# Optimization experiments

Measured on AMD Instinct MI355X. Metric: run time of the kernel, lower is better.

## Reference

```python
import jax, jax.numpy as jnp
import numpy as np
from jax import lax

NC1, NC2, NC3 = 64, 64, 512
TEMP = 1.0
EPS = 1e-5
B = 256


def setup_inputs() -> dict:
    key = jax.random.key(0)
    ks = jax.random.split(key, 16)
    d = {}
    d["inp"] = jax.random.normal(ks[0], (B, 3, 32, 32), jnp.float32)
    d["conv1_w"] = jax.random.normal(ks[1], (6, 3, 5, 5), jnp.float32) * 0.1
    d["conv1_b"] = jax.random.normal(ks[2], (6,), jnp.float32) * 0.1
    d["bn1_g"] = jnp.ones((6,), jnp.float32)
    d["bn1_b"] = jnp.zeros((6,), jnp.float32)
    d["conv2_w"] = jax.random.normal(ks[3], (16, 6, 5, 5), jnp.float32) * 0.1
    d["conv2_b"] = jax.random.normal(ks[4], (16,), jnp.float32) * 0.1
    d["bn2_g"] = jnp.ones((16,), jnp.float32)
    d["bn2_b"] = jnp.zeros((16,), jnp.float32)
    d["fc1_w"] = jax.random.normal(ks[5], (120, 400), jnp.float32) * 0.05
    d["fc1_b"] = jax.random.normal(ks[6], (120,), jnp.float32) * 0.05
    d["fc2_w"] = jax.random.normal(ks[7], (10, 120), jnp.float32) * 0.05
    d["fc2_b"] = jax.random.normal(ks[8], (10,), jnp.float32) * 0.05
    d["k1s"] = jax.random.normal(ks[9], (NC1, 6), jnp.float32)
    d["k2s"] = jax.random.normal(ks[10], (NC2, 16), jnp.float32)
    d["k3s"] = jax.random.normal(ks[11], (NC3, 120), jnp.float32)
    return d


def _conv(x, w, b):
    y = lax.conv_general_dilated(x, w, (1, 1), 'VALID',
                                 dimension_numbers=('NCHW', 'OIHW', 'NCHW'))
    return y + b[None, :, None, None]


def _bn_train(x, g, b):
    # BatchNorm2d in training mode: biased batch stats over (N,H,W)
    mean = x.mean(axis=(0, 2, 3), keepdims=True)
    var = ((x - mean) ** 2).mean(axis=(0, 2, 3), keepdims=True)
    return (x - mean) / jnp.sqrt(var + EPS) * g[None, :, None, None] + b[None, :, None, None]


def _maxpool2(x):
    return lax.reduce_window(x, -jnp.inf, lax.max, (1, 1, 2, 2), (1, 1, 2, 2), 'VALID')


def _codebook_logits_spatial(act, keys):
    # act: [B,C,H,W], keys: [K,C] -> -||act - k||_2 over C -> [B,K,H,W]
    diff = act[:, None] - keys[None, :, :, None, None]
    return -jnp.sqrt((diff ** 2).sum(axis=2))


def _neural_gas_loss(v, temp):
    n_clusters = v.shape[1]
    weightings = jnp.exp(-jnp.arange(n_clusters, dtype=v.dtype) / temp)
    sorted_v = jnp.sort(v, axis=1)
    return (sorted_v ** 2 * weightings).sum(axis=1)


def reference(inp, conv1_w, conv1_b, bn1_g, bn1_b, conv2_w, conv2_b, bn2_g, bn2_b,
              fc1_w, fc1_b, fc2_w, fc2_b, k1s, k2s, k3s):
    act1 = _bn_train(_conv(inp, conv1_w, conv1_b), bn1_g, bn1_b)          # [B,6,28,28]
    act_logits1 = _codebook_logits_spatial(act1, k1s)                     # [B,NC1,28,28]
    x = _maxpool2(jax.nn.relu(act1))                                      # [B,6,14,14]
    act2 = _bn_train(_conv(x, conv2_w, conv2_b), bn2_g, bn2_b)            # [B,16,10,10]
    act_logits2 = _codebook_logits_spatial(act2, k2s)                     # [B,NC2,10,10]
    x = _maxpool2(jax.nn.relu(act2))                                      # [B,16,5,5]
    x = x.reshape(x.shape[0], -1)                                         # [B,400]
    act3 = x @ fc1_w.T + fc1_b                                            # [B,120]
    diff3 = act3[:, None, :] - k3s[None, :, :]
    act_logits3 = -jnp.sqrt((diff3 ** 2).sum(axis=2))                     # [B,NC3]
    x = jax.nn.relu(act3)
    act4 = x @ fc2_w.T + fc2_b                                            # [B,10]
    # ARGS.ng branch: neural-gas cluster loss + argmax assignments
    cluster_loss = _neural_gas_loss(act_logits3, TEMP)                    # [B]
    assignments = jnp.argmax(act_logits3, axis=1)                         # [B] int
    return (assignments, cluster_loss.mean(), act4, act_logits1, act_logits2, act_logits3)
```

## Files before the change

kernel.cpp:

```cpp
#include <hip/hip_runtime.h>

#define B 256
#define EPSV 1e-5f

#define OFF_ASSIGN 0
#define OFF_LOSS   256
#define OFF_ACT4   257
#define OFF_L1     2817
#define OFF_L2     12847873
#define OFF_L3     14486273

__device__ inline void wave_reduce2(float& s, float& q) {
#pragma unroll
    for (int o = 32; o > 0; o >>= 1) {
        s += __shfl_down(s, o, 64);
        q += __shfl_down(q, o, 64);
    }
}

__global__ __launch_bounds__(256) void conv1_kernel(
        const float* __restrict__ inp, const float* __restrict__ w,
        const float* __restrict__ bias, float* __restrict__ c1,
        float* __restrict__ part,
        const float* __restrict__ w1, const float* __restrict__ k3,
        float* __restrict__ w1t, float* __restrict__ k3st) {
    int bc = blockIdx.x;
    int tid = threadIdx.x;
    if (bc >= 1536) {
        int idx = (bc - 1536) * 256 + tid;
        if (idx < 48000) {
            int c = idx / 120, o = idx % 120;
            w1t[idx] = w1[o * 400 + c];
        } else if (idx < 48000 + 61440) {
            int j = idx - 48000;
            int c = j >> 9, k = j & 511;
            k3st[j] = k3[k * 120 + c];
        }
        return;
    }
    int b = bc / 6, c = bc % 6;
    __shared__ float ws[75];
    __shared__ float rs[4], rq[4];
    if (tid < 75) ws[tid] = w[c * 75 + tid];
    __syncthreads();
    const float* ip = inp + b * 3072;
    float bs = bias[c];
    float s = 0.f, sq = 0.f;
    for (int hw = tid; hw < 784; hw += 256) {
        int oh = hw / 28, ow = hw % 28;
        float acc = bs;
#pragma unroll
        for (int ic = 0; ic < 3; ++ic) {
            const float* ipc = ip + ic * 1024 + oh * 32 + ow;
            const float* wc = ws + ic * 25;
#pragma unroll
            for (int kh = 0; kh < 5; ++kh)
#pragma unroll
                for (int kw = 0; kw < 5; ++kw)
                    acc += ipc[kh * 32 + kw] * wc[kh * 5 + kw];
        }
        c1[bc * 784 + hw] = acc;
        s += acc; sq += acc * acc;
    }
    wave_reduce2(s, sq);
    if ((tid & 63) == 0) { rs[tid >> 6] = s; rq[tid >> 6] = sq; }
    __syncthreads();
    if (tid == 0) {
        part[bc * 2]     = rs[0] + rs[1] + rs[2] + rs[3];
        part[bc * 2 + 1] = rq[0] + rq[1] + rq[2] + rq[3];
    }
}

__global__ __launch_bounds__(1024) void stage1_kernel(
        const float* __restrict__ c1raw, const float* __restrict__ part1,
        const float* __restrict__ g1, const float* __restrict__ bb1,
        const float* __restrict__ k1s,
        const float* __restrict__ c2w, const float* __restrict__ c2b,
        float* __restrict__ outL1, float* __restrict__ c2,
        float* __restrict__ part2) {
    int b = blockIdx.x, tid = threadIdx.x;
    int lane = tid & 63, wid = tid >> 6;
    __shared__ float act[4704];
    __shared__ float sk[384];
    __shared__ float w2s[2400];
    __shared__ float xp[1176];
    __shared__ float sa[1600];
    __shared__ float chs[6], chq[6], ssc[6], ssh[6];
    if (wid < 6) {
        float s = 0.f, q = 0.f;
#pragma unroll
        for (int j = 0; j < 4; ++j) {
            int bi = lane + 64 * j;
            s += part1[(bi * 6 + wid) * 2];
            q += part1[(bi * 6 + wid) * 2 + 1];
        }
        wave_reduce2(s, q);
        if (lane == 0) { chs[wid] = s; chq[wid] = q; }
    }
    for (int i = tid; i < 384; i += 1024) sk[i] = k1s[i];
    for (int i = tid; i < 2400; i += 1024) w2s[i] = c2w[i];
    __syncthreads();
    if (tid < 6) {
        float m = chs[tid] * (1.f / 200704.f);
        float v = chq[tid] * (1.f / 200704.f) - m * m;
        float sc = g1[tid] * rsqrtf(v + EPSV);
        ssc[tid] = sc; ssh[tid] = bb1[tid] - m * sc;
    }
    __syncthreads();
    const float* cp = c1raw + b * 4704;
    for (int i = tid; i < 4704; i += 1024) {
        int c = i / 784;
        act[i] = cp[i] * ssc[c] + ssh[c];
    }
    __syncthreads();
    float* op = outL1 + (long)b * 50176;
    for (int i = tid; i < 50176; i += 1024) {
        int k = i / 784, hw = i - k * 784;
        const float* kp = sk + k * 6;
        float d0 = act[hw] - kp[0];
        float d1 = act[784 + hw] - kp[1];
        float d2 = act[1568 + hw] - kp[2];
        float d3 = act[2352 + hw] - kp[3];
        float d4 = act[3136 + hw] - kp[4];
        float d5 = act[3920 + hw] - kp[5];
        float s = d0 * d0 + d1 * d1 + d2 * d2 + d3 * d3 + d4 * d4 + d5 * d5;
        op[i] = -sqrtf(s);
    }
    for (int i = tid; i < 1176; i += 1024) {
        int c = i / 196, p = i % 196, ph = p / 14, pw = p % 14;
        const float* ap = act + c * 784 + ph * 56 + pw * 2;
        float m = fmaxf(fmaxf(ap[0], ap[1]), fmaxf(ap[28], ap[29]));
        xp[i] = fmaxf(m, 0.f);
    }
    __syncthreads();
    for (int i = tid; i < 1600; i += 1024) {
        int c = i / 100, hw = i - c * 100;
        int oh = hw / 10, ow = hw - oh * 10;
        float acc = c2b[c];
#pragma unroll
        for (int ic = 0; ic < 6; ++ic) {
            const float* xsrc = xp + ic * 196 + oh * 14 + ow;
            const float* wp = w2s + c * 150 + ic * 25;
#pragma unroll
            for (int kh = 0; kh < 5; ++kh)
#pragma unroll
                for (int kw = 0; kw < 5; ++kw)
                    acc += xsrc[kh * 14 + kw] * wp[kh * 5 + kw];
        }
        sa[i] = acc;
    }
    __syncthreads();
    for (int i = tid; i < 1600; i += 1024) c2[b * 1600 + i] = sa[i];
    {
        float s = 0.f, q = 0.f;
        if (lane < 100) { float x = sa[wid * 100 + lane]; s = x; q = x * x; }
        if (lane < 36)  { float x = sa[wid * 100 + 64 + lane]; s += x; q += x * x; }
        wave_reduce2(s, q);
        if (lane == 0) {
            part2[(b * 16 + wid) * 2]     = s;
            part2[(b * 16 + wid) * 2 + 1] = q;
        }
    }
}

__global__ __launch_bounds__(1024) void stage2_kernel(
        const float* __restrict__ c2, const float* __restrict__ part2,
        const float* __restrict__ g2, const float* __restrict__ bb2,
        const float* __restrict__ k2s,
        const float* __restrict__ w1t, const float* __restrict__ f1b,
        const float* __restrict__ f2w, const float* __restrict__ f2b,
        const float* __restrict__ k3st,
        float* __restrict__ outL2, float* __restrict__ outAct4,
        float* __restrict__ outL3, float* __restrict__ outAssign,
        float* __restrict__ lossb) {
    int b = blockIdx.x, tid = threadIdx.x;
    int lane = tid & 63, wid = tid >> 6;
    __shared__ float sa[1600];
    __shared__ float sk[1024];
    __shared__ float xs[400];
    __shared__ float chs[16], chq[16], ssc[16], ssh[16];
    __shared__ float partq[8][128];
    __shared__ float a3r[120], a3p[120];
    __shared__ float pv[2][512];
    __shared__ float sv[512];
    __shared__ int   cntp[2][512];
    __shared__ float wsum[8], wmv[8];
    __shared__ int wmi[8];
    {
        float s = 0.f, q = 0.f;
#pragma unroll
        for (int j = 0; j < 4; ++j) {
            int bi = lane + 64 * j;
            s += part2[(bi * 16 + wid) * 2];
            q += part2[(bi * 16 + wid) * 2 + 1];
        }
        wave_reduce2(s, q);
        if (lane == 0) { chs[wid] = s; chq[wid] = q; }
    }
    for (int i = tid; i < 1024; i += 1024) sk[i] = k2s[i];
    __syncthreads();
    if (tid < 16) {
        float m = chs[tid] * (1.f / 25600.f);
        float v = chq[tid] * (1.f / 25600.f) - m * m;
        float sc = g2[tid] * rsqrtf(v + EPSV);
        ssc[tid] = sc; ssh[tid] = bb2[tid] - m * sc;
    }
    __syncthreads();
    for (int i = tid; i < 1600; i += 1024) {
        int c = i / 100;
        sa[i] = c2[b * 1600 + i] * ssc[c] + ssh[c];
    }
    __syncthreads();
    float* op2 = outL2 + (long)b * 6400;
    for (int i = tid; i < 6400; i += 1024) {
        int k = i / 100, hw = i - k * 100;
        float s = 0.f;
#pragma unroll
        for (int c = 0; c < 16; ++c) {
            float d = sa[c * 100 + hw] - sk[k * 16 + c];
            s += d * d;
        }
        op2[i] = -sqrtf(s);
    }
    for (int i = tid; i < 400; i += 1024) {
        int c = i / 25, p = i % 25, ph = p / 5, pw = p % 5;
        const float* ap = sa + c * 100 + ph * 20 + pw * 2;
        float m = fmaxf(fmaxf(ap[0], ap[1]), fmaxf(ap[10], ap[11]));
        xs[i] = fmaxf(m, 0.f);
    }
    __syncthreads();
    {
        int o = tid & 127, q8 = tid >> 7;
        float s = 0.f;
        if (o < 120) {
            const float* wp = w1t + (q8 * 50) * 120 + o;
            const float* xp2 = xs + q8 * 50;
#pragma unroll 10
            for (int c = 0; c < 50; ++c) s += xp2[c] * wp[c * 120];
        }
        partq[q8][o] = s;
    }
    __syncthreads();
    if (tid < 120) {
        float acc = f1b[tid];
#pragma unroll
        for (int q8 = 0; q8 < 8; ++q8) acc += partq[q8][tid];
        a3r[tid] = acc;
        a3p[tid] = fmaxf(acc, 0.f);
    }
    __syncthreads();
    {
        int k = tid & 511, h = tid >> 9;
        const float* kp = k3st + k;
        float s = 0.f;
#pragma unroll 10
        for (int c = 0; c < 60; ++c) {
            int cc = h * 60 + c;
            float d = a3r[cc] - kp[cc * 512];
            s += d * d;
        }
        pv[h][k] = s;
    }
    if (tid < 10) {
        float acc = f2b[tid];
        const float* wp = f2w + tid * 120;
#pragma unroll 8
        for (int c = 0; c < 120; ++c) acc += a3p[c] * wp[c];
        outAct4[b * 10 + tid] = acc;
    }
    __syncthreads();
    if (tid < 512) {
        float v = -sqrtf(pv[0][tid] + pv[1][tid]);
        sv[tid] = v;
        outL3[(long)b * 512 + tid] = v;
    }
    __syncthreads();
    {
        int i = tid & 511, h = tid >> 9;
        float v = sv[i];
        const float4* sv4 = reinterpret_cast<const float4*>(sv);
        int cnt = 0;
#pragma unroll 8
        for (int j4 = h * 64; j4 < h * 64 + 64; ++j4) {
            float4 o4 = sv4[j4];
            int jb = j4 * 4;
            cnt += (o4.x < v || (o4.x == v && jb < i)) ? 1 : 0;
            cnt += (o4.y < v || (o4.y == v && jb + 1 < i)) ? 1 : 0;
            cnt += (o4.z < v || (o4.z == v && jb + 2 < i)) ? 1 : 0;
            cnt += (o4.w < v || (o4.w == v && jb + 3 < i)) ? 1 : 0;
        }
        cntp[h][i] = cnt;
    }
    __syncthreads();
    if (tid < 512) {
        float v = sv[tid];
        int cnt = cntp[0][tid] + cntp[1][tid];
        float contrib = v * v * expf(-(float)cnt);
        float ssum = contrib;
#pragma unroll
        for (int o = 32; o > 0; o >>= 1) ssum += __shfl_down(ssum, o, 64);
        float mv = v; int mi = tid;
#pragma unroll
        for (int o = 32; o > 0; o >>= 1) {
            float ov = __shfl_down(mv, o, 64);
            int oi = __shfl_down(mi, o, 64);
            if (ov > mv || (ov == mv && oi < mi)) { mv = ov; mi = oi; }
        }
        if (lane == 0) { wsum[wid] = ssum; wmv[wid] = mv; wmi[wid] = mi; }
    }
    __syncthreads();
    if (tid == 0) {
        float tot = 0.f;
        float bmv = wmv[0]; int bmi = wmi[0];
#pragma unroll
        for (int w = 0; w < 8; ++w) {
            tot += wsum[w];
            if (wmv[w] > bmv || (wmv[w] == bmv && wmi[w] < bmi)) { bmv = wmv[w]; bmi = wmi[w]; }
        }
        lossb[b] = tot;
        outAssign[b] = (float)bmi;
    }
}

__global__ void final_kernel(const float* __restrict__ loss_b, float* __restrict__ out_loss) {
    __shared__ float r[256];
    int tid = threadIdx.x;
    r[tid] = loss_b[tid];
    __syncthreads();
    for (int s = 128; s > 0; s >>= 1) {
        if (tid < s) r[tid] += r[tid + s];
        __syncthreads();
    }
    if (tid == 0) out_loss[0] = r[0] / 256.f;
}

extern "C" void kernel_launch(void* const* d_in, const int* in_sizes, int n_in,
                              void* d_out, int out_size, void* d_ws, size_t ws_size,
                              hipStream_t stream) {
    const float* inp = (const float*)d_in[0];
    const float* c1w = (const float*)d_in[1];
    const float* c1b = (const float*)d_in[2];
    const float* g1  = (const float*)d_in[3];
    const float* bb1 = (const float*)d_in[4];
    const float* c2w = (const float*)d_in[5];
    const float* c2b = (const float*)d_in[6];
    const float* g2  = (const float*)d_in[7];
    const float* bb2 = (const float*)d_in[8];
    const float* f1w = (const float*)d_in[9];
    const float* f1b = (const float*)d_in[10];
    const float* f2w = (const float*)d_in[11];
    const float* f2b = (const float*)d_in[12];
    const float* k1  = (const float*)d_in[13];
    const float* k2  = (const float*)d_in[14];
    const float* k3  = (const float*)d_in[15];
    float* out = (float*)d_out;

    float* W = (float*)d_ws;
    float* c1raw = W;
    float* part1 = c1raw + 1204224;
    float* c2raw = part1 + 3072;
    float* part2 = c2raw + 409600;
    float* lossb = part2 + 8192;
    float* w1t   = lossb + 256;
    float* k3st  = w1t + 48000;

    conv1_kernel<<<1964, 256, 0, stream>>>(inp, c1w, c1b, c1raw, part1,
                                           f1w, k3, w1t, k3st);
    stage1_kernel<<<B, 1024, 0, stream>>>(c1raw, part1, g1, bb1, k1, c2w, c2b,
                                          out + OFF_L1, c2raw, part2);
    stage2_kernel<<<B, 1024, 0, stream>>>(c2raw, part2, g2, bb2, k2,
                                          w1t, f1b, f2w, f2b, k3st,
                                          out + OFF_L2, out + OFF_ACT4,
                                          out + OFF_L3, out + OFF_ASSIGN, lossb);
    final_kernel<<<1, 256, 0, stream>>>(lossb, out + OFF_LOSS);
}
```

Measured before the change: 94.49 us.

## Use norm expansion for codebook distances and overlap pooling with logit computation

Codebook distances are now computed as ||a||^2 + ||k||^2 - 2 a·k, clamped at zero. Each thread keeps one pixel's activations in registers and loops over the codebook entries, while a separate set of threads does the max-pooling at the same time. The conv2 output is written to global memory directly instead of in a second pass. This cuts per-element subtraction work and index division, and lets the pooling threads run alongside the logit threads. In exchange it may lose floating-point accuracy when distances are small, through cancellation, and each thread's stores now stride by plane instead of being fully contiguous across iterations.

Result: faster. 91.79 us (-2.9%).

```diff
diff --git a/kernel.cpp b/kernel.cpp
--- a/kernel.cpp
+++ b/kernel.cpp
@@ -10,7 +10,7 @@
 #define OFF_L2     12847873
 #define OFF_L3     14486273
 
-__device__ inline void wave_reduce2(float& s, float& q) {
+__device__ __forceinline__ void wave_reduce2(float& s, float& q) {
 #pragma unroll
     for (int o = 32; o > 0; o >>= 1) {
         s += __shfl_down(s, o, 64);
@@ -76,15 +76,15 @@
         const float* __restrict__ g1, const float* __restrict__ bb1,
         const float* __restrict__ k1s,
         const float* __restrict__ c2w, const float* __restrict__ c2b,
-        float* __restrict__ outL1, float* __restrict__ c2,
+        float* __restrict__ out, float* __restrict__ c2raw,
         float* __restrict__ part2) {
     int b = blockIdx.x, tid = threadIdx.x;
     int lane = tid & 63, wid = tid >> 6;
-    __shared__ float act[4704];
-    __shared__ float sk[384];
+    __shared__ __align__(16) float act[4704];
+    __shared__ float sk1[384], k2sq1[64];
     __shared__ float w2s[2400];
     __shared__ float xp[1176];
-    __shared__ float sa[1600];
+    __shared__ __align__(16) float sa[1600];
     __shared__ float chs[6], chq[6], ssc[6], ssh[6];
     if (wid < 6) {
         float s = 0.f, q = 0.f;
@@ -97,7 +97,7 @@
         wave_reduce2(s, q);
         if (lane == 0) { chs[wid] = s; chq[wid] = q; }
     }
-    for (int i = tid; i < 384; i += 1024) sk[i] = k1s[i];
+    if (tid >= 640 && tid < 1024) sk1[tid - 640] = k1s[tid - 640];
     for (int i = tid; i < 2400; i += 1024) w2s[i] = c2w[i];
     __syncthreads();
     if (tid < 6) {
@@ -106,31 +106,38 @@
         float sc = g1[tid] * rsqrtf(v + EPSV);
         ssc[tid] = sc; ssh[tid] = bb1[tid] - m * sc;
     }
-    __syncthreads();
-    const float* cp = c1raw + b * 4704;
+    if (tid >= 64 && tid < 128) {
+        int k = tid - 64;
+        float s = 0.f;
+#pragma unroll
+        for (int c = 0; c < 6; ++c) { float x = sk1[k * 6 + c]; s += x * x; }
+        k2sq1[k] = s;
+    }
+    __syncthreads();
     for (int i = tid; i < 4704; i += 1024) {
         int c = i / 784;
-        act[i] = cp[i] * ssc[c] + ssh[c];
-    }
-    __syncthreads();
-    float* op = outL1 + (long)b * 50176;
-    for (int i = tid; i < 50176; i += 1024) {
-        int k = i / 784, hw = i - k * 784;
-        const float* kp = sk + k * 6;
-        float d0 = act[hw] - kp[0];
-        float d1 = act[784 + hw] - kp[1];
-        float d2 = act[1568 + hw] - kp[2];
-        float d3 = act[2352 + hw] - kp[3];
-        float d4 = act[3136 + hw] - kp[4];
-        float d5 = act[3920 + hw] - kp[5];
-        float s = d0 * d0 + d1 * d1 + d2 * d2 + d3 * d3 + d4 * d4 + d5 * d5;
-        op[i] = -sqrtf(s);
-    }
-    for (int i = tid; i < 1176; i += 1024) {
-        int c = i / 196, p = i % 196, ph = p / 14, pw = p % 14;
-        const float* ap = act + c * 784 + ph * 56 + pw * 2;
-        float m = fmaxf(fmaxf(ap[0], ap[1]), fmaxf(ap[28], ap[29]));
-        xp[i] = fmaxf(m, 0.f);
+        act[i] = c1raw[b * 4704 + i] * ssc[c] + ssh[c];
+    }
+    __syncthreads();
+    if (tid < 784) {
+        float a0 = act[tid], a1 = act[784 + tid], a2 = act[1568 + tid];
+        float a3 = act[2352 + tid], a4 = act[3136 + tid], a5 = act[3920 + tid];
+        float A2 = a0*a0 + a1*a1 + a2*a2 + a3*a3 + a4*a4 + a5*a5;
+        float* op = out + OFF_L1 + (long)b * 50176 + tid;
+#pragma unroll 4
+        for (int k = 0; k < 64; ++k) {
+            const float* kp = sk1 + k * 6;
+            float dot = a0*kp[0] + a1*kp[1] + a2*kp[2] + a3*kp[3] + a4*kp[4] + a5*kp[5];
+            *op = -sqrtf(fmaxf(A2 + k2sq1[k] - 2.f * dot, 0.f));
+            op += 784;
+        }
+    } else {
+        for (int i = tid - 784; i < 1176; i += 240) {
+            int c = i / 196, p = i % 196, ph = p / 14, pw = p % 14;
+            const float* ap = act + c * 784 + ph * 56 + pw * 2;
+            float m = fmaxf(fmaxf(ap[0], ap[1]), fmaxf(ap[28], ap[29]));
+            xp[i] = fmaxf(m, 0.f);
+        }
     }
     __syncthreads();
     for (int i = tid; i < 1600; i += 1024) {
@@ -148,42 +155,37 @@
                     acc += xsrc[kh * 14 + kw] * wp[kh * 5 + kw];
         }
         sa[i] = acc;
-    }
-    __syncthreads();
-    for (int i = tid; i < 1600; i += 1024) c2[b * 1600 + i] = sa[i];
+        c2raw[b * 1600 + i] = acc;
+    }
+    __syncthreads();
     {
         float s = 0.f, q = 0.f;
         if (lane < 100) { float x = sa[wid * 100 + lane]; s = x; q = x * x; }
         if (lane < 36)  { float x = sa[wid * 100 + 64 + lane]; s += x; q += x * x; }
         wave_reduce2(s, q);
-        if (lane == 0) {
-            part2[(b * 16 + wid) * 2]     = s;
-            part2[(b * 16 + wid) * 2 + 1] = q;
-        }
+        if (lane == 0) { part2[(b * 16 + wid) * 2] = s; part2[(b * 16 + wid) * 2 + 1] = q; }
     }
 }
 
 __global__ __launch_bounds__(1024) void stage2_kernel(
-        const float* __restrict__ c2, const float* __restrict__ part2,
+        const float* __restrict__ c2raw, const float* __restrict__ part2,
         const float* __restrict__ g2, const float* __restrict__ bb2,
         const float* __restrict__ k2s,
         const float* __restrict__ w1t, const float* __restrict__ f1b,
         const float* __restrict__ f2w, const float* __restrict__ f2b,
         const float* __restrict__ k3st,
-        float* __restrict__ outL2, float* __restrict__ outAct4,
-        float* __restrict__ outL3, float* __restrict__ outAssign,
-        float* __restrict__ lossb) {
+        float* __restrict__ out, float* __restrict__ lossb) {
     int b = blockIdx.x, tid = threadIdx.x;
     int lane = tid & 63, wid = tid >> 6;
-    __shared__ float sa[1600];
-    __shared__ float sk[1024];
+    __shared__ __align__(16) float sa[1600];
+    __shared__ float sk2[1024], k2sq2[64];
+    __shared__ float chs[16], chq[16], ssc[16], ssh[16];
     __shared__ float xs[400];
-    __shared__ float chs[16], chq[16], ssc[16], ssh[16];
-    __shared__ float partq[8][128];
+    __shared__ float partq[1024];
     __shared__ float a3r[120], a3p[120];
-    __shared__ float pv[2][512];
-    __shared__ float sv[512];
-    __shared__ int   cntp[2][512];
+    __shared__ __align__(16) float sv[512];
+    __shared__ __align__(16) float pv[1024];
+    __shared__ int cntp[1024];
     __shared__ float wsum[8], wmv[8];
     __shared__ int wmi[8];
     {
@@ -197,7 +199,7 @@
         wave_reduce2(s, q);
         if (lane == 0) { chs[wid] = s; chq[wid] = q; }
     }
-    for (int i = tid; i < 1024; i += 1024) sk[i] = k2s[i];
+    sk2[tid] = k2s[tid];
     __syncthreads();
     if (tid < 16) {
         float m = chs[tid] * (1.f / 25600.f);
@@ -205,28 +207,41 @@
         float sc = g2[tid] * rsqrtf(v + EPSV);
         ssc[tid] = sc; ssh[tid] = bb2[tid] - m * sc;
     }
+    if (tid >= 64 && tid < 128) {
+        int k = tid - 64;
+        float s = 0.f;
+#pragma unroll
+        for (int c = 0; c < 16; ++c) { float x = sk2[k * 16 + c]; s += x * x; }
+        k2sq2[k] = s;
+    }
     __syncthreads();
     for (int i = tid; i < 1600; i += 1024) {
         int c = i / 100;
-        sa[i] = c2[b * 1600 + i] * ssc[c] + ssh[c];
-    }
-    __syncthreads();
-    float* op2 = outL2 + (long)b * 6400;
-    for (int i = tid; i < 6400; i += 1024) {
-        int k = i / 100, hw = i - k * 100;
-        float s = 0.f;
-#pragma unroll
-        for (int c = 0; c < 16; ++c) {
-            float d = sa[c * 100 + hw] - sk[k * 16 + c];
-            s += d * d;
-        }
-        op2[i] = -sqrtf(s);
-    }
-    for (int i = tid; i < 400; i += 1024) {
-        int c = i / 25, p = i % 25, ph = p / 5, pw = p % 5;
-        const float* ap = sa + c * 100 + ph * 20 + pw * 2;
-        float m = fmaxf(fmaxf(ap[0], ap[1]), fmaxf(ap[10], ap[11]));
-        xs[i] = fmaxf(m, 0.f);
+        sa[i] = c2raw[b * 1600 + i] * ssc[c] + ssh[c];
+    }
+    __syncthreads();
+    if (tid < 800) {
+        int kg = tid / 100, hw = tid - kg * 100;
+        float a[16], A2 = 0.f;
+#pragma unroll
+        for (int c = 0; c < 16; ++c) { a[c] = sa[c * 100 + hw]; A2 += a[c] * a[c]; }
+        float* op2 = out + OFF_L2 + (long)b * 6400 + kg * 800 + hw;
+#pragma unroll
+        for (int k = kg * 8; k < kg * 8 + 8; ++k) {
+            const float* kp = sk2 + k * 16;
+            float dot = 0.f;
+#pragma unroll
+            for (int c = 0; c < 16; ++c) dot += a[c] * kp[c];
+            *op2 = -sqrtf(fmaxf(A2 + k2sq2[k] - 2.f * dot, 0.f));
+            op2 += 100;
+        }
+    } else {
+        for (int i = tid - 800; i < 400; i += 224) {
+            int c = i / 25, p = i % 25, ph = p / 5, pw = p % 5;
+            const float* ap = sa + c * 100 + ph * 20 + pw * 2;
+            float m = fmaxf(fmaxf(ap[0], ap[1]), fmaxf(ap[10], ap[11]));
+            xs[i] = fmaxf(m, 0.f);
+        }
     }
     __syncthreads();
     {
@@ -234,17 +249,17 @@
         float s = 0.f;
         if (o < 120) {
             const float* wp = w1t + (q8 * 50) * 120 + o;
-            const float* xp2 = xs + q8 * 50;
+            const float* xq = xs + q8 * 50;
 #pragma unroll 10
-            for (int c = 0; c < 50; ++c) s += xp2[c] * wp[c * 120];
-        }
-        partq[q8][o] = s;
+            for (int c = 0; c < 50; ++c) s += xq[c] * wp[c * 120];
+        }
+        partq[q8 * 128 + o] = s;
     }
     __syncthreads();
     if (tid < 120) {
         float acc = f1b[tid];
 #pragma unroll
-        for (int q8 = 0; q8 < 8; ++q8) acc += partq[q8][tid];
+        for (int q8 = 0; q8 < 8; ++q8) acc += partq[q8 * 128 + tid];
         a3r[tid] = acc;
         a3p[tid] = fmaxf(acc, 0.f);
     }
@@ -253,26 +268,25 @@
         int k = tid & 511, h = tid >> 9;
         const float* kp = k3st + k;
         float s = 0.f;
-#pragma unroll 10
-        for (int c = 0; c < 60; ++c) {
-            int cc = h * 60 + c;
-            float d = a3r[cc] - kp[cc * 512];
+#pragma unroll 6
+        for (int c = h * 60; c < h * 60 + 60; ++c) {
+            float d = a3r[c] - kp[c * 512];
             s += d * d;
         }
-        pv[h][k] = s;
+        pv[h * 512 + k] = s;
     }
     if (tid < 10) {
         float acc = f2b[tid];
         const float* wp = f2w + tid * 120;
 #pragma unroll 8
         for (int c = 0; c < 120; ++c) acc += a3p[c] * wp[c];
-        outAct4[b * 10 + tid] = acc;
+        out[OFF_ACT4 + b * 10 + tid] = acc;
     }
     __syncthreads();
     if (tid < 512) {
-        float v = -sqrtf(pv[0][tid] + pv[1][tid]);
+        float v = -sqrtf(pv[tid] + pv[512 + tid]);
         sv[tid] = v;
-        outL3[(long)b * 512 + tid] = v;
+        out[OFF_L3 + (long)b * 512 + tid] = v;
     }
     __syncthreads();
     {
@@ -289,12 +303,12 @@
             cnt += (o4.z < v || (o4.z == v && jb + 2 < i)) ? 1 : 0;
             cnt += (o4.w < v || (o4.w == v && jb + 3 < i)) ? 1 : 0;
         }
-        cntp[h][i] = cnt;
+        cntp[h * 512 + i] = cnt;
     }
     __syncthreads();
     if (tid < 512) {
         float v = sv[tid];
-        int cnt = cntp[0][tid] + cntp[1][tid];
+        int cnt = cntp[tid] + cntp[512 + tid];
         float contrib = v * v * expf(-(float)cnt);
         float ssum = contrib;
 #pragma unroll
@@ -318,7 +332,7 @@
             if (wmv[w] > bmv || (wmv[w] == bmv && wmi[w] < bmi)) { bmv = wmv[w]; bmi = wmi[w]; }
         }
         lossb[b] = tot;
-        outAssign[b] = (float)bmi;
+        out[OFF_ASSIGN + b] = (float)bmi;
     }
 }
 
@@ -367,10 +381,8 @@
     conv1_kernel<<<1964, 256, 0, stream>>>(inp, c1w, c1b, c1raw, part1,
                                            f1w, k3, w1t, k3st);
     stage1_kernel<<<B, 1024, 0, stream>>>(c1raw, part1, g1, bb1, k1, c2w, c2b,
-                                          out + OFF_L1, c2raw, part2);
+                                          out, c2raw, part2);
     stage2_kernel<<<B, 1024, 0, stream>>>(c2raw, part2, g2, bb2, k2,
-                                          w1t, f1b, f2w, f2b, k3st,
-                                          out + OFF_L2, out + OFF_ACT4,
-                                          out + OFF_L3, out + OFF_ASSIGN, lossb);
+                                          w1t, f1b, f2w, f2b, k3st, out, lossb);
     final_kernel<<<1, 256, 0, stream>>>(lossb, out + OFF_LOSS);
 }
```
